# Kernel tuning notes

Hardware: AMD Instinct MI355X
Metric: run time of the kernel (lower is better)

Reference implementation:

```python
import jax, jax.numpy as jnp
import numpy as np

ALPHA, BETA, GAMMA = 1.0, 1.0, 0.7
WIN = 11
C1 = 0.01 ** 2
C2 = 0.03 ** 2


def get_sobel_kernels(n1=1, n2=2, n3=2):
    a = np.asarray
    Sx = a([[[-n1, 0, n1], [-n2, 0, n2], [-n1, 0, n1]],
            [[-n2, 0, n2], [-n3 * n2, 0, n3 * n2], [-n2, 0, n2]],
            [[-n1, 0, n1], [-n2, 0, n2], [-n1, 0, n1]]])
    Sy = a([[[-n1, -n2, -n1], [0, 0, 0], [n1, n2, n1]],
            [[-n2, -n3 * n2, -n2], [0, 0, 0], [n2, n3 * n2, n2]],
            [[-n1, -n2, -n1], [0, 0, 0], [n1, n2, n1]]])
    Sz = a([[[-n1, -n2, -n1], [-n2, -n3 * n2, -n2], [-n1, -n2, -n1]],
            [[0, 0, 0], [0, 0, 0], [0, 0, 0]],
            [[n1, n2, n1], [n2, n3 * n2, n2], [n1, n2, n1]]])
    Sd11 = a([[[0, n1, n2], [-n1, 0, n1], [-n2, -n1, 0]],
              [[0, n2, n2 * n3], [-n2, 0, n2], [-n2 * n3, -n2, 0]],
              [[0, n1, n2], [-n1, 0, n1], [-n2, -n1, 0]]])
    Sd12 = a([[[-n2, -n1, 0], [-n1, 0, n1], [0, n1, n2]],
              [[-n2 * n3, -n2, 0], [-n2, 0, n2], [0, n2, n2 * n3]],
              [[-n2, -n1, 0], [-n1, 0, n1], [0, n1, n2]]])
    Sd21 = Sd11.T
    Sd22 = Sd12.T
    Sd31 = a([-S.T for S in Sd11.T])
    Sd32 = a([S.T for S in Sd12.T])
    return np.stack([Sx, Sy, Sz, Sd11, Sd12, Sd21, Sd22, Sd31, Sd32]).astype(np.float32)

# (9,1,3,3,3) fused sobel bank -- single grouped conv instead of 9 launches
SOBEL_W = jnp.asarray(get_sobel_kernels()[:, None])


def _gauss1d():
    g = jnp.exp(-(jnp.arange(WIN, dtype=jnp.float32) - WIN // 2) ** 2 / (2 * 1.5 ** 2))
    return g / g.sum()

G1D = _gauss1d()


def conv3d(x, w):
    return jax.lax.conv_general_dilated(
        x, w, window_strides=(1, 1, 1), padding='SAME',
        dimension_numbers=('NCDHW', 'OIDHW', 'NCDHW'))


def gauss_filter(x):
    # separable 11-tap gaussian along D, H, W (== full 11^3 window, zero-padded SAME)
    x = conv3d(x, G1D.reshape(1, 1, WIN, 1, 1))
    x = conv3d(x, G1D.reshape(1, 1, 1, WIN, 1))
    x = conv3d(x, G1D.reshape(1, 1, 1, 1, WIN))
    return x


def edge_map(img):
    # GradEdge3D.__call__ with a=1, C=1
    B, C, D, H, W = img.shape
    xp = jnp.pad(img, ((0, 0), (0, 0), (1, 1), (1, 1), (1, 1)), mode='reflect')
    g = conv3d(xp, SOBEL_W)                       # (B, 9, D+2, H+2, W+2)
    gm = jnp.sqrt(jnp.sum((g + 1e-6) ** 2 + 1e-6, axis=1))  # (B, D+2, H+2, W+2)
    gm = gm[:, 1:-1, 1:-1, 1:-1]
    norm = (gm - gm.min()) / (gm.max() - gm.min() + 1e-6)
    return norm.reshape(B, 1, D, H, W)


def ssim_value(pred, target):
    mu_p = gauss_filter(pred)
    mu_t = gauss_filter(target)
    mu_p2, mu_t2, mu_pt = mu_p ** 2, mu_t ** 2, mu_p * mu_t
    sig_p = gauss_filter(pred * pred) - mu_p2
    sig_t = gauss_filter(target * target) - mu_t2
    sig_pt = gauss_filter(pred * target) - mu_pt
    ssim_map = ((2 * mu_pt + C1) * (2 * sig_pt + C2)) / ((mu_p2 + mu_t2 + C1) * (sig_p + sig_t + C2))
    return 1.0 - ssim_map.mean()


def setup_inputs() -> dict:
    key = jax.random.key(0)
    k1, k2 = jax.random.split(key)
    shape = (2, 1, 128, 128, 128)
    return {
        'pred': jax.random.uniform(k1, shape, dtype=jnp.float32),
        'target': jax.random.uniform(k2, shape, dtype=jnp.float32),
    }


def reference(pred, target):
    loss_mse = jnp.mean((pred - target) ** 2)
    loss_ssim = ssim_value(pred, target)
    # GMELoss3D: lam_errors=[(1.0, L1Loss())], reduction='sum'
    loss_gme = 1e-6 + jnp.mean(jnp.abs(edge_map(pred) - edge_map(target)))
    total = ALPHA * loss_mse + BETA * loss_ssim + GAMMA * loss_gme
    return (total, loss_mse, loss_ssim, loss_gme)
```

## Files before the change

kernel.cpp:

```cpp
#include <hip/hip_runtime.h>


#define VOL 4194304
#define HV  2097152

typedef _Float16 h2 __attribute__((ext_vector_type(2)));
typedef _Float16 h4 __attribute__((ext_vector_type(4)));
typedef _Float16 h8 __attribute__((ext_vector_type(8)));

constexpr float GW[11] = {
    0.00102838f, 0.00759876f, 0.03600077f, 0.10936070f, 0.21300554f,
    0.26601173f,
    0.21300554f, 0.10936070f, 0.03600077f, 0.00759876f, 0.00102838f};


__device__ __forceinline__ void wblur_body(
    const float* __restrict__ p, const float* __restrict__ t,
    _Float16* __restrict__ A, double* __restrict__ mseS, const int unit,
    char* __restrict__ pool, float* __restrict__ redw) {
  float (* __restrict__ sr)[140] = (float (*)[140])pool;
  float (* __restrict__ dr)[140] = (float (*)[140])(pool + 8960);
  const int tid = threadIdx.x;
  const int gbase = unit << 11;
  if (tid < 192) {
    const int r = tid / 12, j = tid % 12;
    const int c = (j < 6) ? j : (128 + j);
    sr[r][c] = 0.f; dr[r][c] = 0.f;
  }
  float msel = 0.f;
  const float2* __restrict__ p2 = (const float2*)(p + gbase);
  const float2* __restrict__ t2 = (const float2*)(t + gbase);
#pragma unroll
  for (int i = 0; i < 4; ++i) {
    const int u = (i << 8) + tid;
    const int row = u >> 6, xp = u & 63;
    const float2 pv = p2[u];
    const float2 tv = t2[u];
    const float s0 = pv.x + tv.x, d0 = pv.x - tv.x;
    const float s1 = pv.y + tv.y, d1 = pv.y - tv.y;
    msel += d0 * d0;
    msel += d1 * d1;
    *(float2*)&sr[row][6 + (xp << 1)] = make_float2(s0, s1);
    *(float2*)&dr[row][6 + (xp << 1)] = make_float2(d0, d1);
  }
  __syncthreads();
  h8* __restrict__ A8 = (h8*)A;
#pragma unroll
  for (int i = 0; i < 4; ++i) {
    const int u = (i << 8) + tid;
    const int row = u >> 6, x0 = (u & 63) << 1;
    float as0 = 0.f, ad0 = 0.f, ass0 = 0.f, add0 = 0.f;
    float as1 = 0.f, ad1 = 0.f, ass1 = 0.f, add1 = 0.f;
#pragma unroll
    for (int k = 0; k < 11; ++k) {
      const float w = GW[k];
      const float a0 = sr[row][1 + x0 + k];
      const float b0 = dr[row][1 + x0 + k];
      const float wa0 = w * a0, wb0 = w * b0;
      as0 += wa0; ad0 += wb0; ass0 += wa0 * a0; add0 += wb0 * b0;
      const float a1 = sr[row][2 + x0 + k];
      const float b1 = dr[row][2 + x0 + k];
      const float wa1 = w * a1, wb1 = w * b1;
      as1 += wa1; ad1 += wb1; ass1 += wa1 * a1; add1 += wb1 * b1;
    }
    h8 o;
    o[0] = (_Float16)as0;  o[1] = (_Float16)ad0;
    o[2] = (_Float16)ass0; o[3] = (_Float16)add0;
    o[4] = (_Float16)as1;  o[5] = (_Float16)ad1;
    o[6] = (_Float16)ass1; o[7] = (_Float16)add1;
    A8[(gbase >> 1) + u] = o;
  }
  redw[tid] = msel;
  __syncthreads();
  for (int s = 128; s > 0; s >>= 1) {
    if (tid < s) redw[tid] += redw[tid + s];
    __syncthreads();
  }
  if (tid == 0) mseS[unit] = (double)redw[0];
}

__device__ __forceinline__ void sobel_body(
    const float* __restrict__ p, const float* __restrict__ t,
    _Float16* __restrict__ gmP, _Float16* __restrict__ gmT,
    float* __restrict__ fminS, float* __restrict__ fmaxS,
    const int bx, const int by, const int bz, const int sidx,
    char* __restrict__ pool, float* __restrict__ rmin) {
  float* __restrict__ sb   = (float*)pool;
  float* __restrict__ rmax = (float*)(pool + 5184);
  const int tid = threadIdx.x;
  const int tx = tid & 15;
  const int ty = tid >> 4;
  const int x0 = bx << 4;
  const int y0 = by << 4;
  const int vol = bz >> 3;
  const int b   = (bz >> 2) & 1;
  const int z0  = (bz & 3) << 5;
  const float* __restrict__ img = vol ? t : p;
  _Float16* __restrict__ gm = vol ? gmT : gmP;
  const int vb = b << 21;

  const int ly1 = tid / 24, lx1 = tid % 24;
  const bool v1 = (lx1 < 18);
  int gy1 = y0 - 1 + ly1; gy1 = gy1 < 0 ? 1 : (gy1 > 127 ? 126 : gy1);
  int gx1 = x0 - 1 + lx1; gx1 = gx1 < 0 ? 1 : (gx1 > 127 ? 126 : gx1);
  const int off1 = (gy1 << 7) + gx1;
  const int s2i = tid + 256;
  const int ly2 = s2i / 24, lx2 = s2i % 24;
  const bool v2 = (s2i < 432) && (lx2 < 18);
  int gy2 = y0 - 1 + ly2; gy2 = gy2 < 0 ? 1 : (gy2 > 127 ? 126 : gy2);
  int gx2 = x0 - 1 + lx2; gx2 = gx2 < 0 ? 1 : (gx2 > 127 ? 126 : gx2);
  const int off2 = (gy2 << 7) + gx2;
  const int rb = ty * 24 + tx;
  const int gbase = vb + (z0 << 14) + ((y0 + ty) << 7) + (x0 + tx);

  float Y0[7], Y1[7], Y2[7];
  float rv1 = 0.f, rv2 = 0.f;
  float lmin = 3.4e38f, lmax = 0.f;

#define LOADR(ZS) {                                                         \
    const int zc_ = (ZS) > 127 ? 126 : (ZS);                                \
    const int za_ = vb + (zc_ << 14);                                       \
    if (v1) rv1 = img[za_ + off1];                                          \
    if (v2) rv2 = img[za_ + off2]; }

#define WRITELDS(BOFF) {                                                    \
    if (v1) sb[(BOFF) + tid] = rv1;                                         \
    if (v2) sb[(BOFF) + s2i] = rv2; }

#define COMPY(P) {                                                          \
    const int o_ = (P) * 432 + rb;                                          \
    const float r00 = sb[o_],      r01 = sb[o_ + 1],  r02 = sb[o_ + 2];     \
    const float r10 = sb[o_ + 24], r11 = sb[o_ + 25], r12 = sb[o_ + 26];    \
    const float r20 = sb[o_ + 48], r21 = sb[o_ + 49], r22 = sb[o_ + 50];    \
    const float dx0 = r02 - r00, dx1 = r12 - r10, dx2 = r22 - r20;          \
    const float ux0 = r00 + r01 + r02, ux1 = r10 + r11 + r12,               \
                ux2 = r20 + r21 + r22;                                      \
    const float sx0 = ux0 + r01, sx1 = ux1 + r11, sx2 = ux2 + r21;          \
    Y##P[1] = dx0 + dx1 + dx2;                                    \
    Y##P[0] = Y##P[1] + dx1;                                      \
    Y##P[2] = sx2 - sx0;                                          \
    Y##P[4] = sx0 + sx1 + sx2;                                    \
    Y##P[3] = Y##P[4] + sx1;                                      \
    Y##P[5] = ux2 - ux0;                                          \
    Y##P[6] = (ux0 + ux2) + 2.f * ux1; }

#define EMIT(I, P0, P1, P2) {                                               \
    const float E_ = Y##P0[0] + Y##P1[0] + Y##P2[0];                        \
    const float g1 = E_ + Y##P1[0];                                         \
    const float tA = Y##P0[1] + Y##P1[1] + Y##P2[1];                        \
    const float A_ = tA + Y##P1[1];                                         \
    const float D_ = Y##P0[2] + Y##P1[2] + Y##P2[2];                        \
    const float g2 = D_ + Y##P1[2];                                         \
    const float g3 = Y##P2[3] - Y##P0[3];                                   \
    const float C_ = Y##P2[4] - Y##P0[4];                                   \
    const float B_ = (Y##P0[5] + Y##P2[5]) + 2.f * Y##P1[5];                \
    const float F_ = Y##P2[6] - Y##P0[6];                                   \
    const float g4 = A_ - B_, g5 = A_ + B_;                                 \
    const float g6 = C_ - D_, g7 = C_ + D_;                                 \
    const float g8 = E_ - F_, g9 = E_ + F_;                                 \
    float ss_ = 9e-6f, t_;                                                  \
    t_ = g1 + 1e-6f; ss_ = fmaf(t_, t_, ss_);                               \
    t_ = g2 + 1e-6f; ss_ = fmaf(t_, t_, ss_);                               \
    t_ = g3 + 1e-6f; ss_ = fmaf(t_, t_, ss_);                               \
    t_ = g4 + 1e-6f; ss_ = fmaf(t_, t_, ss_);                               \
    t_ = g5 + 1e-6f; ss_ = fmaf(t_, t_, ss_);                               \
    t_ = g6 + 1e-6f; ss_ = fmaf(t_, t_, ss_);                               \
    t_ = g7 + 1e-6f; ss_ = fmaf(t_, t_, ss_);                               \
    t_ = g8 + 1e-6f; ss_ = fmaf(t_, t_, ss_);                               \
    t_ = g9 + 1e-6f; ss_ = fmaf(t_, t_, ss_);                               \
    const _Float16 gh = (_Float16)sqrtf(ss_);                               \
    gm[gbase + ((I) << 14)] = gh;                                           \
    const float gq = (float)gh;                                             \
    lmin = fminf(lmin, gq); lmax = fmaxf(lmax, gq); }

#define BODY(I, P0, P1, P2) {                                               \
    WRITELDS((P2) * 432);                                                   \
    LOADR(z0 + (I) + 2);                                                    \
    __syncthreads();                                                        \
    COMPY(P2);                                                              \
    EMIT(I, P0, P1, P2); }

  {
    const int zp = (z0 == 0) ? 1 : (z0 - 1);
    LOADR(zp);  WRITELDS(0);
    LOADR(z0);  WRITELDS(432);
    __syncthreads();
    COMPY(0);
    COMPY(1);
    LOADR(z0 + 1);
  }
  for (int ii = 0; ii < 30; ii += 3) {
    BODY(ii,     0, 1, 2);
    BODY(ii + 1, 1, 2, 0);
    BODY(ii + 2, 2, 0, 1);
  }
  BODY(30, 0, 1, 2);
  BODY(31, 1, 2, 0);

#undef BODY
#undef EMIT
#undef COMPY
#undef WRITELDS
#undef LOADR

  rmin[tid] = lmin; rmax[tid] = lmax;
  __syncthreads();
  for (int st = 128; st > 0; st >>= 1) {
    if (tid < st) {
      rmin[tid] = fminf(rmin[tid], rmin[tid + st]);
      rmax[tid] = fmaxf(rmax[tid], rmax[tid + st]);
    }
    __syncthreads();
  }
  if (tid == 0) {
    fminS[sidx] = rmin[0];
    fmaxS[sidx] = rmax[0];
  }
}

__global__ __launch_bounds__(256) void k_fused_a(
    const float* __restrict__ p, const float* __restrict__ t,
    _Float16* __restrict__ A, double* __restrict__ mseS,
    _Float16* __restrict__ gmP, _Float16* __restrict__ gmT,
    float* __restrict__ fminS, float* __restrict__ fmaxS) {
  __shared__ __align__(16) char pool[17920];
  __shared__ float redshared[256];
  const int bid = blockIdx.x;
  const int wg = ((bid & 7) * 384) + (bid >> 3);
  const int r3 = wg % 3;
  const int grp = wg / 3;
  if (r3 < 2) {
    wblur_body(p, t, A, mseS, grp * 2 + r3, pool, redshared);
  } else {
    const int b   = grp >> 9;
    const int z0c = (grp >> 7) & 3;
    const int vol = (grp >> 6) & 1;
    const int by  = (grp >> 3) & 7;
    const int bx  = grp & 7;
    const int bz  = (vol << 3) + (b << 2) + z0c;
    const int sidx = (vol << 9) + (b << 8) + (z0c << 6) + (by << 3) + bx;
    sobel_body(p, t, gmP, gmT, fminS, fmaxS, bx, by, bz, sidx,
               pool, redshared);
  }
}

__global__ __launch_bounds__(256) void k_fused_b(
    const _Float16* __restrict__ A, _Float16* __restrict__ B) {
  const int bid = blockIdx.x;
  const int wg = ((bid & 7) << 8) + (bid >> 3);
  const int yseg = wg & 7;
  const int z = (wg >> 3) & 127;
  const int batch = wg >> 10;
  const int tid = threadIdx.x;
  const int xc = tid & 63;
  const int yg = tid >> 6;
  const h8* __restrict__ Ah = (const h8*)A;
  h8* __restrict__ Bh = (h8*)B;
  const int slice8 = (batch << 20) + (z << 13);
  const int ybase = (yseg << 4) + (yg << 2);
  h8 acc0{}, acc1{}, acc2{}, acc3{};
#pragma unroll
  for (int k = 0; k < 14; ++k) {
    const int y = ybase - 5 + k;
    h8 rv{};
    if ((unsigned)y < 128u) rv = Ah[slice8 + (y << 6) + xc];
    if (k <= 10)           acc0 += (_Float16)GW[k]      * rv;
    if (k >= 1 && k <= 11) acc1 += (_Float16)GW[k - 1]  * rv;
    if (k >= 2 && k <= 12) acc2 += (_Float16)GW[k - 2]  * rv;
    if (k >= 3)            acc3 += (_Float16)GW[k - 3]  * rv;
  }
  const int wbase = slice8 + (ybase << 6) + xc;
  Bh[wbase]            = acc0;
  Bh[wbase + (1 << 6)] = acc1;
  Bh[wbase + (2 << 6)] = acc2;
  Bh[wbase + (3 << 6)] = acc3;
}

__device__ __forceinline__ void edge_body(
    const _Float16* __restrict__ gmP, const _Float16* __restrict__ gmT,
    const float* __restrict__ fminS, const float* __restrict__ fmaxS,
    double* __restrict__ absS, const int bidx,
    float* __restrict__ scr, float* __restrict__ rede) {
  float* __restrict__ rm0 = scr;
  float* __restrict__ rM0 = scr + 256;
  float* __restrict__ rm1 = scr + 512;
  float* __restrict__ rM1 = scr + 768;
  const int tid = threadIdx.x;
  float mnp = 3.4e38f, mxp = 0.f, mnt = 3.4e38f, mxt = 0.f;
  for (int j = tid; j < 512; j += 256) {
    mnp = fminf(mnp, fminS[j]);
    mxp = fmaxf(mxp, fmaxS[j]);
    mnt = fminf(mnt, fminS[512 + j]);
    mxt = fmaxf(mxt, fmaxS[512 + j]);
  }
  rm0[tid] = mnp; rM0[tid] = mxp; rm1[tid] = mnt; rM1[tid] = mxt;
  __syncthreads();
  for (int s = 128; s > 0; s >>= 1) {
    if (tid < s) {
      rm0[tid] = fminf(rm0[tid], rm0[tid + s]);
      rM0[tid] = fmaxf(rM0[tid], rM0[tid + s]);
      rm1[tid] = fminf(rm1[tid], rm1[tid + s]);
      rM1[tid] = fmaxf(rM1[tid], rM1[tid + s]);
    }
    __syncthreads();
  }
  mnp = rm0[0]; mxp = rM0[0]; mnt = rm1[0]; mxt = rM1[0];
  const float scp = 1.f / (mxp - mnp + 1e-6f);
  const float sct = 1.f / (mxt - mnt + 1e-6f);
  const h8* __restrict__ gp = (const h8*)gmP;
  const h8* __restrict__ gt = (const h8*)gmT;
  float lsum = 0.f;
  const int base = bidx << 9;
#pragma unroll
  for (int i = 0; i < 2; ++i) {
    const int idx = base + (i << 8) + tid;
    const h8 a = gp[idx];
    const h8 b = gt[idx];
#pragma unroll
    for (int j = 0; j < 8; ++j)
      lsum += fabsf(((float)a[j] - mnp) * scp - ((float)b[j] - mnt) * sct);
  }
  rede[tid] = lsum;
  __syncthreads();
  for (int s = 128; s > 0; s >>= 1) {
    if (tid < s) rede[tid] += rede[tid + s];
    __syncthreads();
  }
  if (tid == 0) absS[bidx] = (double)rede[0];
}

__global__ __launch_bounds__(256) void k_zblur_ssim(
    const _Float16* __restrict__ B, double* __restrict__ ssimS,
    const _Float16* __restrict__ gmP, const _Float16* __restrict__ gmT,
    const float* __restrict__ fminS, const float* __restrict__ fmaxS,
    double* __restrict__ absS) {
  __shared__ float scr[1024];
  __shared__ float red[256];
  const int tid = threadIdx.x;
  const int bid = blockIdx.x;
  const int wg = ((bid & 7) * 384) + (bid >> 3);
  const int r3 = wg % 3;
  if (r3 == 2) {
    edge_body(gmP, gmT, fminS, fmaxS, absS, wg / 3, scr, red);
    return;
  }
  const int idx = (wg / 3) * 2 + r3;
  const int zseg = idx & 7;
  const int y = (idx >> 3) & 127;
  const int batch = idx >> 10;
  const int xc = tid & 63;
  const int zg = tid >> 6;
  const h8* __restrict__ Bh = (const h8*)B;
  const int col8 = (batch << 20) + (y << 6);
  const int zbase = (zseg << 4) + (zg << 2);
  h8 m0{}, m1{}, m2{}, m3{};
#pragma unroll
  for (int k = 0; k < 14; ++k) {
    const int zz = zbase - 5 + k;
    h8 rv{};
    if ((unsigned)zz < 128u) rv = Bh[col8 + (zz << 13) + xc];
    if (k <= 10)           m0 += (_Float16)GW[k]      * rv;
    if (k >= 1 && k <= 11) m1 += (_Float16)GW[k - 1]  * rv;
    if (k >= 2 && k <= 12) m2 += (_Float16)GW[k - 2]  * rv;
    if (k >= 3)            m3 += (_Float16)GW[k - 3]  * rv;
  }
  float lsum = 0.f;
  h8 mv[4] = {m0, m1, m2, m3};
#pragma unroll
  for (int r = 0; r < 4; ++r) {
#pragma unroll
    for (int j = 0; j < 2; ++j) {
      const float mus = (float)mv[r][4 * j + 0];
      const float mud = (float)mv[r][4 * j + 1];
      const float ess = (float)mv[r][4 * j + 2];
      const float edd = (float)mv[r][4 * j + 3];
      const float S2 = mus * mus, D2 = mud * mud;
      const float num = ((S2 - D2) * 0.5f + 1e-4f) *
                        ((ess - edd - S2 + D2) * 0.5f + 9e-4f);
      const float den = ((S2 + D2) * 0.5f + 1e-4f) *
                        ((ess + edd - S2 - D2) * 0.5f + 9e-4f);
      lsum += num / den;
    }
  }
  red[tid] = lsum;
  __syncthreads();
  for (int st = 128; st > 0; st >>= 1) {
    if (tid < st) red[tid] += red[tid + st];
    __syncthreads();
  }
  if (tid == 0) ssimS[idx] = (double)red[0];
}

__global__ __launch_bounds__(256) void k_final(
    const double* __restrict__ mseS, const double* __restrict__ ssimS,
    const double* __restrict__ absS, float* __restrict__ out) {
  __shared__ double dred[256];
  const int tid = threadIdx.x;
  double msl = 0.0, ssl = 0.0, abl = 0.0;
  for (int j = tid; j < 2048; j += 256) { msl += mseS[j]; ssl += ssimS[j]; }
  for (int j = tid; j < 1024; j += 256) abl += absS[j];
  dred[tid] = msl; __syncthreads();
  for (int s = 128; s > 0; s >>= 1) {
    if (tid < s) dred[tid] += dred[tid + s];
    __syncthreads();
  }
  const double ms = dred[0]; __syncthreads();
  dred[tid] = ssl; __syncthreads();
  for (int s = 128; s > 0; s >>= 1) {
    if (tid < s) dred[tid] += dred[tid + s];
    __syncthreads();
  }
  const double ss = dred[0]; __syncthreads();
  dred[tid] = abl; __syncthreads();
  for (int s = 128; s > 0; s >>= 1) {
    if (tid < s) dred[tid] += dred[tid + s];
    __syncthreads();
  }
  if (tid == 0) {
    const double ab = dred[0];
    const double N = 4194304.0;
    const double mse   = ms / N;
    const double ssiml = 1.0 - ss / N;
    const double gme   = 1e-6 + ab / N;
    const double total = mse + ssiml + 0.7 * gme;
    out[0] = (float)total;
    out[1] = (float)mse;
    out[2] = (float)ssiml;
    out[3] = (float)gme;
  }
}

extern "C" void kernel_launch(void* const* d_in, const int* in_sizes, int n_in,
                              void* d_out, int out_size, void* d_ws, size_t ws_size,
                              hipStream_t stream) {
  const float* p = (const float*)d_in[0];
  const float* t = (const float*)d_in[1];
  _Float16* A = (_Float16*)d_ws;
  _Float16* B = A + (size_t)4 * VOL;
  char* accb = (char*)d_ws + (size_t)20 * VOL;
  double* mseS  = (double*)accb;
  double* ssimS = (double*)(accb + 16384);
  double* absS  = (double*)(accb + 32768);
  float*  fminS = (float*)(accb + 40960);
  float*  fmaxS = (float*)(accb + 45056);
  _Float16* gmP = (_Float16*)((char*)d_ws + 88080384);
  _Float16* gmT = gmP + VOL;
  float* out = (float*)d_out;

  k_fused_a<<<3072, 256, 0, stream>>>(p, t, A, mseS, gmP, gmT, fminS, fmaxS);
  k_fused_b<<<2048, 256, 0, stream>>>(A, B);
  k_zblur_ssim<<<3072, 256, 0, stream>>>(B, ssimS, gmP, gmT, fminS, fmaxS,
                                         absS);
  k_final<<<1, 256, 0, stream>>>(mseS, ssimS, absS, out);
}
```

Measured before the change: 137.6 us.

## Rebalance work split: shorter sobel z-chunks, taller z-blur tiles per thread

```diff
diff --git a/kernel.cpp b/kernel.cpp
--- a/kernel.cpp
+++ b/kernel.cpp
@@ -92,9 +92,9 @@
   const int ty = tid >> 4;
   const int x0 = bx << 4;
   const int y0 = by << 4;
-  const int vol = bz >> 3;
-  const int b   = (bz >> 2) & 1;
-  const int z0  = (bz & 3) << 5;
+  const int vol = bz >> 4;
+  const int b   = (bz >> 3) & 1;
+  const int z0  = (bz & 7) << 4;
   const float* __restrict__ img = vol ? t : p;
   _Float16* __restrict__ gm = vol ? gmT : gmP;
   const int vb = b << 21;
@@ -189,13 +189,12 @@
     COMPY(1);
     LOADR(z0 + 1);
   }
-  for (int ii = 0; ii < 30; ii += 3) {
+  for (int ii = 0; ii < 15; ii += 3) {
     BODY(ii,     0, 1, 2);
     BODY(ii + 1, 1, 2, 0);
     BODY(ii + 2, 2, 0, 1);
   }
-  BODY(30, 0, 1, 2);
-  BODY(31, 1, 2, 0);
+  BODY(15, 0, 1, 2);
 
 #undef BODY
 #undef EMIT
@@ -226,19 +225,19 @@
   __shared__ __align__(16) char pool[17920];
   __shared__ float redshared[256];
   const int bid = blockIdx.x;
-  const int wg = ((bid & 7) * 384) + (bid >> 3);
-  const int r3 = wg % 3;
-  const int grp = wg / 3;
-  if (r3 < 2) {
-    wblur_body(p, t, A, mseS, grp * 2 + r3, pool, redshared);
+  const int wg = ((bid & 7) << 9) + (bid >> 3);
+  if ((wg & 1) == 0) {
+    wblur_body(p, t, A, mseS, wg >> 1, pool, redshared);
   } else {
-    const int b   = grp >> 9;
-    const int z0c = (grp >> 7) & 3;
-    const int vol = (grp >> 6) & 1;
-    const int by  = (grp >> 3) & 7;
-    const int bx  = grp & 7;
-    const int bz  = (vol << 3) + (b << 2) + z0c;
-    const int sidx = (vol << 9) + (b << 8) + (z0c << 6) + (by << 3) + bx;
+    const int s = wg >> 1;
+    const int b   = s >> 10;
+    const int rem = s & 1023;
+    const int z0c = rem >> 7;
+    const int vol = (rem >> 6) & 1;
+    const int by  = (rem >> 3) & 7;
+    const int bx  = rem & 7;
+    const int bz  = (vol << 4) + (b << 3) + z0c;
+    const int sidx = (vol << 10) + (b << 9) + (z0c << 6) + (by << 3) + bx;
     sobel_body(p, t, gmP, gmT, fminS, fmaxS, bx, by, bz, sidx,
                pool, redshared);
   }
@@ -287,11 +286,11 @@
   float* __restrict__ rM1 = scr + 768;
   const int tid = threadIdx.x;
   float mnp = 3.4e38f, mxp = 0.f, mnt = 3.4e38f, mxt = 0.f;
-  for (int j = tid; j < 512; j += 256) {
+  for (int j = tid; j < 1024; j += 256) {
     mnp = fminf(mnp, fminS[j]);
     mxp = fmaxf(mxp, fmaxS[j]);
-    mnt = fminf(mnt, fminS[512 + j]);
-    mxt = fmaxf(mxt, fmaxS[512 + j]);
+    mnt = fminf(mnt, fminS[1024 + j]);
+    mxt = fmaxf(mxt, fmaxS[1024 + j]);
   }
   rm0[tid] = mnp; rM0[tid] = mxp; rm1[tid] = mnt; rM1[tid] = mxt;
   __syncthreads();
@@ -338,42 +337,39 @@
   __shared__ float red[256];
   const int tid = threadIdx.x;
   const int bid = blockIdx.x;
-  const int wg = ((bid & 7) * 384) + (bid >> 3);
-  const int r3 = wg % 3;
-  if (r3 == 2) {
-    edge_body(gmP, gmT, fminS, fmaxS, absS, wg / 3, scr, red);
+  const int wg = ((bid & 7) << 8) + (bid >> 3);
+  if (wg & 1) {
+    edge_body(gmP, gmT, fminS, fmaxS, absS, wg >> 1, scr, red);
     return;
   }
-  const int idx = (wg / 3) * 2 + r3;
-  const int zseg = idx & 7;
-  const int y = (idx >> 3) & 127;
-  const int batch = idx >> 10;
+  const int u = wg >> 1;
+  const int zseg = u & 3;
+  const int y = (u >> 2) & 127;
+  const int batch = u >> 9;
   const int xc = tid & 63;
   const int zg = tid >> 6;
   const h8* __restrict__ Bh = (const h8*)B;
   const int col8 = (batch << 20) + (y << 6);
-  const int zbase = (zseg << 4) + (zg << 2);
-  h8 m0{}, m1{}, m2{}, m3{};
-#pragma unroll
-  for (int k = 0; k < 14; ++k) {
+  const int zbase = (zseg << 5) + (zg << 3);
+  h8 m[8] = {};
+#pragma unroll
+  for (int k = 0; k < 18; ++k) {
     const int zz = zbase - 5 + k;
     h8 rv{};
     if ((unsigned)zz < 128u) rv = Bh[col8 + (zz << 13) + xc];
-    if (k <= 10)           m0 += (_Float16)GW[k]      * rv;
-    if (k >= 1 && k <= 11) m1 += (_Float16)GW[k - 1]  * rv;
-    if (k >= 2 && k <= 12) m2 += (_Float16)GW[k - 2]  * rv;
-    if (k >= 3)            m3 += (_Float16)GW[k - 3]  * rv;
+#pragma unroll
+    for (int r = 0; r < 8; ++r)
+      if (k >= r && k <= r + 10) m[r] += (_Float16)GW[k - r] * rv;
   }
   float lsum = 0.f;
-  h8 mv[4] = {m0, m1, m2, m3};
-#pragma unroll
-  for (int r = 0; r < 4; ++r) {
+#pragma unroll
+  for (int r = 0; r < 8; ++r) {
 #pragma unroll
     for (int j = 0; j < 2; ++j) {
-      const float mus = (float)mv[r][4 * j + 0];
-      const float mud = (float)mv[r][4 * j + 1];
-      const float ess = (float)mv[r][4 * j + 2];
-      const float edd = (float)mv[r][4 * j + 3];
+      const float mus = (float)m[r][4 * j + 0];
+      const float mud = (float)m[r][4 * j + 1];
+      const float ess = (float)m[r][4 * j + 2];
+      const float edd = (float)m[r][4 * j + 3];
       const float S2 = mus * mus, D2 = mud * mud;
       const float num = ((S2 - D2) * 0.5f + 1e-4f) *
                         ((ess - edd - S2 + D2) * 0.5f + 9e-4f);
@@ -388,7 +384,7 @@
     if (tid < st) red[tid] += red[tid + st];
     __syncthreads();
   }
-  if (tid == 0) ssimS[idx] = (double)red[0];
+  if (tid == 0) ssimS[u] = (double)red[0];
 }
 
 __global__ __launch_bounds__(256) void k_final(
@@ -397,8 +393,8 @@
   __shared__ double dred[256];
   const int tid = threadIdx.x;
   double msl = 0.0, ssl = 0.0, abl = 0.0;
-  for (int j = tid; j < 2048; j += 256) { msl += mseS[j]; ssl += ssimS[j]; }
-  for (int j = tid; j < 1024; j += 256) abl += absS[j];
+  for (int j = tid; j < 2048; j += 256) msl += mseS[j];
+  for (int j = tid; j < 1024; j += 256) { ssl += ssimS[j]; abl += absS[j]; }
   dred[tid] = msl; __syncthreads();
   for (int s = 128; s > 0; s >>= 1) {
     if (tid < s) dred[tid] += dred[tid + s];
@@ -440,16 +436,16 @@
   char* accb = (char*)d_ws + (size_t)20 * VOL;
   double* mseS  = (double*)accb;
   double* ssimS = (double*)(accb + 16384);
-  double* absS  = (double*)(accb + 32768);
-  float*  fminS = (float*)(accb + 40960);
-  float*  fmaxS = (float*)(accb + 45056);
+  double* absS  = (double*)(accb + 24576);
+  float*  fminS = (float*)(accb + 32768);
+  float*  fmaxS = (float*)(accb + 40960);
   _Float16* gmP = (_Float16*)((char*)d_ws + 88080384);
   _Float16* gmT = gmP + VOL;
   float* out = (float*)d_out;
 
-  k_fused_a<<<3072, 256, 0, stream>>>(p, t, A, mseS, gmP, gmT, fminS, fmaxS);
+  k_fused_a<<<4096, 256, 0, stream>>>(p, t, A, mseS, gmP, gmT, fminS, fmaxS);
   k_fused_b<<<2048, 256, 0, stream>>>(A, B);
-  k_zblur_ssim<<<3072, 256, 0, stream>>>(B, ssimS, gmP, gmT, fminS, fmaxS,
+  k_zblur_ssim<<<2048, 256, 0, stream>>>(B, ssimS, gmP, gmT, fminS, fmaxS,
                                          absS);
   k_final<<<1, 256, 0, stream>>>(mseS, ssimS, absS, out);
 }
```

Measured after the change: 141.7 us. 3.0% more time.
